# Kernel tuning notes

Measured on AMD Instinct MI355X. Metric: run time of the kernel, lower is better.

The kernel has to match this reference:

```python
import jax, jax.numpy as jnp
import numpy as np

B = 32768
C = 1000


def setup_inputs() -> dict:
    key = jax.random.key(0)
    k1, k2, k3 = jax.random.split(key, 3)
    output = jax.random.normal(k1, (B, C), dtype=jnp.float32)
    target = jax.random.randint(k2, (B,), 0, C, dtype=jnp.int64)
    # loss_lams rows are (approx) probability vectors from the previous epoch
    lams = jax.random.uniform(k3, (C, C), dtype=jnp.float32)
    loss_lams = lams / jnp.sum(lams, axis=1, keepdims=True)
    return {"output": output, "target": target, "loss_lams": loss_lams}


def reference(output, target, loss_lams):
    """OLS loss forward.

    Returns (loss, cur_epoch_lams_update, cur_epoch_cnt_update) where the
    updates are the increments added to the zero-initialized per-epoch state
    (update_loss_lams side effect), and loss = 0.5*CE + 0.5*softCE.
    """
    b, c = output.shape
    target = target.astype(jnp.int32)

    # --- update_loss_lams: softmax, keep samples where argmax == target,
    # scatter-add their prob vectors into the row of their target class ---
    probs = jax.nn.softmax(output, axis=1)                      # [B, C]
    pred = jnp.argmax(probs, axis=1)                            # [B]
    correct = (pred == target).astype(output.dtype)             # [B]
    lams_update = jax.ops.segment_sum(probs * correct[:, None], target,
                                      num_segments=c)           # [C, C]
    cnt_update = jax.ops.segment_sum(correct, target, num_segments=c)  # [C]

    # --- loss: 0.5 * hard CE + 0.5 * soft CE with loss_lams soft labels ---
    log_probs = jax.nn.log_softmax(output, axis=1)              # [B, C]
    ce = -jnp.mean(jnp.take_along_axis(log_probs, target[:, None], axis=1))
    soft_targets = loss_lams[target]                            # [B, C] gather
    soft_ce = -jnp.sum(log_probs * soft_targets) / b
    loss = 0.5 * ce + 0.5 * soft_ce
    return loss, lams_update, cnt_update
```

## Files before the change

kernel.cpp:

```cpp
#include <hip/hip_runtime.h>
#include <math.h>

constexpr int B_ROWS = 32768;
constexpr int C_COLS = 1000;
constexpr int VEC4   = C_COLS / 4;

__global__ __launch_bounds__(256) void ols_loss_kernel(
    const float* __restrict__ output,
    const int*   __restrict__ target,
    const float* __restrict__ lams,
    float*       __restrict__ d_loss,
    float*       __restrict__ lams_upd,
    float*       __restrict__ cnt_upd)
{
    __shared__ float s_loss[4];
    const int lane = threadIdx.x & 63;
    const int wid  = threadIdx.x >> 6;
    const int wavesPerBlock = blockDim.x >> 6;
    const int gwave = blockIdx.x * wavesPerBlock + wid;
    const int nwave = gridDim.x * wavesPerBlock;
    const bool has3 = (lane + 192) < VEC4;

    float lossAcc = 0.0f;

    for (int row = gwave; row < B_ROWS; row += nwave) {
        const float4* xr = reinterpret_cast<const float4*>(output + (size_t)row * C_COLS);
        float4 v0 = xr[lane];
        float4 v1 = xr[lane + 64];
        float4 v2 = xr[lane + 128];
        float4 v3 = has3 ? xr[lane + 192]
                         : make_float4(-INFINITY, -INFINITY, -INFINITY, -INFINITY);

        float m  = v0.x;
        int   am = 4 * lane;
#define OLS_UPD(val, idx) { float _v = (val); if (_v > m) { m = _v; am = (idx); } }
        OLS_UPD(v0.y, 4*lane + 1)  OLS_UPD(v0.z, 4*lane + 2)  OLS_UPD(v0.w, 4*lane + 3)
        OLS_UPD(v1.x, 4*lane + 256) OLS_UPD(v1.y, 4*lane + 257)
        OLS_UPD(v1.z, 4*lane + 258) OLS_UPD(v1.w, 4*lane + 259)
        OLS_UPD(v2.x, 4*lane + 512) OLS_UPD(v2.y, 4*lane + 513)
        OLS_UPD(v2.z, 4*lane + 514) OLS_UPD(v2.w, 4*lane + 515)
        OLS_UPD(v3.x, 4*lane + 768) OLS_UPD(v3.y, 4*lane + 769)
        OLS_UPD(v3.z, 4*lane + 770) OLS_UPD(v3.w, 4*lane + 771)
#undef OLS_UPD

#pragma unroll
        for (int off = 32; off > 0; off >>= 1) {
            float om = __shfl_xor(m, off);
            int   oa = __shfl_xor(am, off);
            if (om > m || (om == m && oa < am)) { m = om; am = oa; }
        }

        float s =
            __expf(v0.x - m) + __expf(v0.y - m) + __expf(v0.z - m) + __expf(v0.w - m) +
            __expf(v1.x - m) + __expf(v1.y - m) + __expf(v1.z - m) + __expf(v1.w - m) +
            __expf(v2.x - m) + __expf(v2.y - m) + __expf(v2.z - m) + __expf(v2.w - m) +
            __expf(v3.x - m) + __expf(v3.y - m) + __expf(v3.z - m) + __expf(v3.w - m);
#pragma unroll
        for (int off = 32; off > 0; off >>= 1) s += __shfl_xor(s, off);

        const float lse = m + __logf(s);

        const int   t   = target[row];
        const float x_t = output[(size_t)row * C_COLS + t];

        const float4* lr = reinterpret_cast<const float4*>(lams + (size_t)t * C_COLS);
        float4 l0 = lr[lane];
        float4 l1 = lr[lane + 64];
        float4 l2 = lr[lane + 128];
        float dot = l0.x*v0.x + l0.y*v0.y + l0.z*v0.z + l0.w*v0.w
                  + l1.x*v1.x + l1.y*v1.y + l1.z*v1.z + l1.w*v1.w
                  + l2.x*v2.x + l2.y*v2.y + l2.z*v2.z + l2.w*v2.w;
        float rs  = l0.x + l0.y + l0.z + l0.w
                  + l1.x + l1.y + l1.z + l1.w
                  + l2.x + l2.y + l2.z + l2.w;
        if (has3) {
            float4 l3 = lr[lane + 192];
            dot += l3.x*v3.x + l3.y*v3.y + l3.z*v3.z + l3.w*v3.w;
            rs  += l3.x + l3.y + l3.z + l3.w;
        }
#pragma unroll
        for (int off = 32; off > 0; off >>= 1) {
            dot += __shfl_xor(dot, off);
            rs  += __shfl_xor(rs,  off);
        }

        if (lane == 0) lossAcc += 0.5f * ((lse - x_t) + (lse * rs - dot));

        if (am == t) {
            const float inv = 1.0f / s;
            float* dst = lams_upd + (size_t)t * C_COLS;
            atomicAdd(&dst[4*lane + 0],   __expf(v0.x - m) * inv);
            atomicAdd(&dst[4*lane + 1],   __expf(v0.y - m) * inv);
            atomicAdd(&dst[4*lane + 2],   __expf(v0.z - m) * inv);
            atomicAdd(&dst[4*lane + 3],   __expf(v0.w - m) * inv);
            atomicAdd(&dst[4*lane + 256], __expf(v1.x - m) * inv);
            atomicAdd(&dst[4*lane + 257], __expf(v1.y - m) * inv);
            atomicAdd(&dst[4*lane + 258], __expf(v1.z - m) * inv);
            atomicAdd(&dst[4*lane + 259], __expf(v1.w - m) * inv);
            atomicAdd(&dst[4*lane + 512], __expf(v2.x - m) * inv);
            atomicAdd(&dst[4*lane + 513], __expf(v2.y - m) * inv);
            atomicAdd(&dst[4*lane + 514], __expf(v2.z - m) * inv);
            atomicAdd(&dst[4*lane + 515], __expf(v2.w - m) * inv);
            if (has3) {
                atomicAdd(&dst[4*lane + 768], __expf(v3.x - m) * inv);
                atomicAdd(&dst[4*lane + 769], __expf(v3.y - m) * inv);
                atomicAdd(&dst[4*lane + 770], __expf(v3.z - m) * inv);
                atomicAdd(&dst[4*lane + 771], __expf(v3.w - m) * inv);
            }
            if (lane == 0) atomicAdd(&cnt_upd[t], 1.0f);
        }
    }

    if (lane == 0) s_loss[wid] = lossAcc;
    __syncthreads();
    if (threadIdx.x == 0) {
        float tot = 0.0f;
        for (int i = 0; i < wavesPerBlock; ++i) tot += s_loss[i];
        atomicAdd(d_loss, tot * (1.0f / (float)B_ROWS));
    }
}

extern "C" void kernel_launch(void* const* d_in, const int* in_sizes, int n_in,
                              void* d_out, int out_size, void* d_ws, size_t ws_size,
                              hipStream_t stream) {
    const float* output = (const float*)d_in[0];
    const int*   target = (const int*)d_in[1];
    const float* lams   = (const float*)d_in[2];

    float* out      = (float*)d_out;
    float* d_loss   = out;
    float* lams_upd = out + 1;
    float* cnt_upd  = out + 1 + C_COLS * C_COLS;

    hipMemsetAsync(d_out, 0, (size_t)out_size * sizeof(float), stream);

    dim3 grid(2048), block(256);
    ols_loss_kernel<<<grid, block, 0, stream>>>(output, target, lams,
                                                d_loss, lams_upd, cnt_upd);
}
```

Measured before the change: 211.6 us.

## Map one row per wave, issue all loads upfront, fetch target logit via shuffle

Replaces the grid-stride loop with one row per wave and a grid of B/4 blocks. The target and lams-row loads are issued before the max reduction so they overlap with the logits loads. Logits use nontemporal loads. The three reductions (sum, dot, rowsum) share one fused shuffle loop, and x_t comes from a register shuffle instead of a dependent global load. This removes serialized load latency per row, at the cost of launching 8192 blocks and one atomic on the loss per block.

New measurement: 275.8 us. 30.3% more time.

```diff
diff --git a/kernel.cpp b/kernel.cpp
--- a/kernel.cpp
+++ b/kernel.cpp
@@ -4,6 +4,8 @@
 constexpr int B_ROWS = 32768;
 constexpr int C_COLS = 1000;
 constexpr int VEC4   = C_COLS / 4;
+
+using f4 = __attribute__((ext_vector_type(4))) float;
 
 __global__ __launch_bounds__(256) void ols_loss_kernel(
     const float* __restrict__ output,
@@ -16,106 +18,106 @@
     __shared__ float s_loss[4];
     const int lane = threadIdx.x & 63;
     const int wid  = threadIdx.x >> 6;
-    const int wavesPerBlock = blockDim.x >> 6;
-    const int gwave = blockIdx.x * wavesPerBlock + wid;
-    const int nwave = gridDim.x * wavesPerBlock;
-    const bool has3 = (lane + 192) < VEC4;
+    const int row  = blockIdx.x * 4 + wid;
+    const bool has3 = lane < (VEC4 - 192);
 
-    float lossAcc = 0.0f;
+    const int t = __builtin_nontemporal_load(target + row);
 
-    for (int row = gwave; row < B_ROWS; row += nwave) {
-        const float4* xr = reinterpret_cast<const float4*>(output + (size_t)row * C_COLS);
-        float4 v0 = xr[lane];
-        float4 v1 = xr[lane + 64];
-        float4 v2 = xr[lane + 128];
-        float4 v3 = has3 ? xr[lane + 192]
-                         : make_float4(-INFINITY, -INFINITY, -INFINITY, -INFINITY);
+    const f4* xr = reinterpret_cast<const f4*>(output + (size_t)row * C_COLS);
+    f4 v0 = __builtin_nontemporal_load(xr + lane);
+    f4 v1 = __builtin_nontemporal_load(xr + lane + 64);
+    f4 v2 = __builtin_nontemporal_load(xr + lane + 128);
+    f4 v3;
+    if (has3) v3 = __builtin_nontemporal_load(xr + lane + 192);
+    else      v3 = (f4){-INFINITY, -INFINITY, -INFINITY, -INFINITY};
 
-        float m  = v0.x;
-        int   am = 4 * lane;
+    const f4* lr = reinterpret_cast<const f4*>(lams + (size_t)t * C_COLS);
+    f4 l0 = lr[lane];
+    f4 l1 = lr[lane + 64];
+    f4 l2 = lr[lane + 128];
+    f4 l3;
+    if (has3) l3 = lr[lane + 192];
+    else      l3 = (f4){0.0f, 0.0f, 0.0f, 0.0f};
+
+    float m  = v0[0];
+    int   am = 4 * lane;
 #define OLS_UPD(val, idx) { float _v = (val); if (_v > m) { m = _v; am = (idx); } }
-        OLS_UPD(v0.y, 4*lane + 1)  OLS_UPD(v0.z, 4*lane + 2)  OLS_UPD(v0.w, 4*lane + 3)
-        OLS_UPD(v1.x, 4*lane + 256) OLS_UPD(v1.y, 4*lane + 257)
-        OLS_UPD(v1.z, 4*lane + 258) OLS_UPD(v1.w, 4*lane + 259)
-        OLS_UPD(v2.x, 4*lane + 512) OLS_UPD(v2.y, 4*lane + 513)
-        OLS_UPD(v2.z, 4*lane + 514) OLS_UPD(v2.w, 4*lane + 515)
-        OLS_UPD(v3.x, 4*lane + 768) OLS_UPD(v3.y, 4*lane + 769)
-        OLS_UPD(v3.z, 4*lane + 770) OLS_UPD(v3.w, 4*lane + 771)
+    OLS_UPD(v0[1], 4*lane + 1)   OLS_UPD(v0[2], 4*lane + 2)   OLS_UPD(v0[3], 4*lane + 3)
+    OLS_UPD(v1[0], 4*lane + 256) OLS_UPD(v1[1], 4*lane + 257)
+    OLS_UPD(v1[2], 4*lane + 258) OLS_UPD(v1[3], 4*lane + 259)
+    OLS_UPD(v2[0], 4*lane + 512) OLS_UPD(v2[1], 4*lane + 513)
+    OLS_UPD(v2[2], 4*lane + 514) OLS_UPD(v2[3], 4*lane + 515)
+    OLS_UPD(v3[0], 4*lane + 768) OLS_UPD(v3[1], 4*lane + 769)
+    OLS_UPD(v3[2], 4*lane + 770) OLS_UPD(v3[3], 4*lane + 771)
 #undef OLS_UPD
 
 #pragma unroll
-        for (int off = 32; off > 0; off >>= 1) {
-            float om = __shfl_xor(m, off);
-            int   oa = __shfl_xor(am, off);
-            if (om > m || (om == m && oa < am)) { m = om; am = oa; }
-        }
-
-        float s =
-            __expf(v0.x - m) + __expf(v0.y - m) + __expf(v0.z - m) + __expf(v0.w - m) +
-            __expf(v1.x - m) + __expf(v1.y - m) + __expf(v1.z - m) + __expf(v1.w - m) +
-            __expf(v2.x - m) + __expf(v2.y - m) + __expf(v2.z - m) + __expf(v2.w - m) +
-            __expf(v3.x - m) + __expf(v3.y - m) + __expf(v3.z - m) + __expf(v3.w - m);
-#pragma unroll
-        for (int off = 32; off > 0; off >>= 1) s += __shfl_xor(s, off);
-
-        const float lse = m + __logf(s);
-
-        const int   t   = target[row];
-        const float x_t = output[(size_t)row * C_COLS + t];
-
-        const float4* lr = reinterpret_cast<const float4*>(lams + (size_t)t * C_COLS);
-        float4 l0 = lr[lane];
-        float4 l1 = lr[lane + 64];
-        float4 l2 = lr[lane + 128];
-        float dot = l0.x*v0.x + l0.y*v0.y + l0.z*v0.z + l0.w*v0.w
-                  + l1.x*v1.x + l1.y*v1.y + l1.z*v1.z + l1.w*v1.w
-                  + l2.x*v2.x + l2.y*v2.y + l2.z*v2.z + l2.w*v2.w;
-        float rs  = l0.x + l0.y + l0.z + l0.w
-                  + l1.x + l1.y + l1.z + l1.w
-                  + l2.x + l2.y + l2.z + l2.w;
-        if (has3) {
-            float4 l3 = lr[lane + 192];
-            dot += l3.x*v3.x + l3.y*v3.y + l3.z*v3.z + l3.w*v3.w;
-            rs  += l3.x + l3.y + l3.z + l3.w;
-        }
-#pragma unroll
-        for (int off = 32; off > 0; off >>= 1) {
-            dot += __shfl_xor(dot, off);
-            rs  += __shfl_xor(rs,  off);
-        }
-
-        if (lane == 0) lossAcc += 0.5f * ((lse - x_t) + (lse * rs - dot));
-
-        if (am == t) {
-            const float inv = 1.0f / s;
-            float* dst = lams_upd + (size_t)t * C_COLS;
-            atomicAdd(&dst[4*lane + 0],   __expf(v0.x - m) * inv);
-            atomicAdd(&dst[4*lane + 1],   __expf(v0.y - m) * inv);
-            atomicAdd(&dst[4*lane + 2],   __expf(v0.z - m) * inv);
-            atomicAdd(&dst[4*lane + 3],   __expf(v0.w - m) * inv);
-            atomicAdd(&dst[4*lane + 256], __expf(v1.x - m) * inv);
-            atomicAdd(&dst[4*lane + 257], __expf(v1.y - m) * inv);
-            atomicAdd(&dst[4*lane + 258], __expf(v1.z - m) * inv);
-            atomicAdd(&dst[4*lane + 259], __expf(v1.w - m) * inv);
-            atomicAdd(&dst[4*lane + 512], __expf(v2.x - m) * inv);
-            atomicAdd(&dst[4*lane + 513], __expf(v2.y - m) * inv);
-            atomicAdd(&dst[4*lane + 514], __expf(v2.z - m) * inv);
-            atomicAdd(&dst[4*lane + 515], __expf(v2.w - m) * inv);
-            if (has3) {
-                atomicAdd(&dst[4*lane + 768], __expf(v3.x - m) * inv);
-                atomicAdd(&dst[4*lane + 769], __expf(v3.y - m) * inv);
-                atomicAdd(&dst[4*lane + 770], __expf(v3.z - m) * inv);
-                atomicAdd(&dst[4*lane + 771], __expf(v3.w - m) * inv);
-            }
-            if (lane == 0) atomicAdd(&cnt_upd[t], 1.0f);
-        }
+    for (int off = 32; off > 0; off >>= 1) {
+        float om = __shfl_xor(m, off);
+        int   oa = __shfl_xor(am, off);
+        if (om > m || (om == m && oa < am)) { m = om; am = oa; }
     }
 
-    if (lane == 0) s_loss[wid] = lossAcc;
+    float dot = l0[0]*v0[0] + l0[1]*v0[1] + l0[2]*v0[2] + l0[3]*v0[3]
+              + l1[0]*v1[0] + l1[1]*v1[1] + l1[2]*v1[2] + l1[3]*v1[3]
+              + l2[0]*v2[0] + l2[1]*v2[1] + l2[2]*v2[2] + l2[3]*v2[3];
+    float rs  = l0[0] + l0[1] + l0[2] + l0[3]
+              + l1[0] + l1[1] + l1[2] + l1[3]
+              + l2[0] + l2[1] + l2[2] + l2[3];
+    if (has3) {
+        dot += l3[0]*v3[0] + l3[1]*v3[1] + l3[2]*v3[2] + l3[3]*v3[3];
+        rs  += l3[0] + l3[1] + l3[2] + l3[3];
+    }
+
+    float s =
+        __expf(v0[0] - m) + __expf(v0[1] - m) + __expf(v0[2] - m) + __expf(v0[3] - m) +
+        __expf(v1[0] - m) + __expf(v1[1] - m) + __expf(v1[2] - m) + __expf(v1[3] - m) +
+        __expf(v2[0] - m) + __expf(v2[1] - m) + __expf(v2[2] - m) + __expf(v2[3] - m) +
+        __expf(v3[0] - m) + __expf(v3[1] - m) + __expf(v3[2] - m) + __expf(v3[3] - m);
+
+#pragma unroll
+    for (int off = 32; off > 0; off >>= 1) {
+        s   += __shfl_xor(s,   off);
+        dot += __shfl_xor(dot, off);
+        rs  += __shfl_xor(rs,  off);
+    }
+
+    const float lse = m + __logf(s);
+
+    const int g = t >> 8, e = t & 3, src_lane = (t >> 2) & 63;
+    f4 vg = (g == 0) ? v0 : (g == 1) ? v1 : (g == 2) ? v2 : v3;
+    float ce = (e == 0) ? vg[0] : (e == 1) ? vg[1] : (e == 2) ? vg[2] : vg[3];
+    const float x_t = __shfl(ce, src_lane, 64);
+
+    if (lane == 0) s_loss[wid] = 0.5f * ((lse - x_t) + (lse * rs - dot));
+
+    if (am == t) {
+        const float inv = 1.0f / s;
+        float* dst = lams_upd + (size_t)t * C_COLS;
+        atomicAdd(&dst[4*lane + 0],   __expf(v0[0] - m) * inv);
+        atomicAdd(&dst[4*lane + 1],   __expf(v0[1] - m) * inv);
+        atomicAdd(&dst[4*lane + 2],   __expf(v0[2] - m) * inv);
+        atomicAdd(&dst[4*lane + 3],   __expf(v0[3] - m) * inv);
+        atomicAdd(&dst[4*lane + 256], __expf(v1[0] - m) * inv);
+        atomicAdd(&dst[4*lane + 257], __expf(v1[1] - m) * inv);
+        atomicAdd(&dst[4*lane + 258], __expf(v1[2] - m) * inv);
+        atomicAdd(&dst[4*lane + 259], __expf(v1[3] - m) * inv);
+        atomicAdd(&dst[4*lane + 512], __expf(v2[0] - m) * inv);
+        atomicAdd(&dst[4*lane + 513], __expf(v2[1] - m) * inv);
+        atomicAdd(&dst[4*lane + 514], __expf(v2[2] - m) * inv);
+        atomicAdd(&dst[4*lane + 515], __expf(v2[3] - m) * inv);
+        if (has3) {
+            atomicAdd(&dst[4*lane + 768], __expf(v3[0] - m) * inv);
+            atomicAdd(&dst[4*lane + 769], __expf(v3[1] - m) * inv);
+            atomicAdd(&dst[4*lane + 770], __expf(v3[2] - m) * inv);
+            atomicAdd(&dst[4*lane + 771], __expf(v3[3] - m) * inv);
+        }
+        if (lane == 0) atomicAdd(&cnt_upd[t], 1.0f);
+    }
+
     __syncthreads();
     if (threadIdx.x == 0) {
-        float tot = 0.0f;
-        for (int i = 0; i < wavesPerBlock; ++i) tot += s_loss[i];
+        float tot = (s_loss[0] + s_loss[1]) + (s_loss[2] + s_loss[3]);
         atomicAdd(d_loss, tot * (1.0f / (float)B_ROWS));
     }
 }
@@ -134,7 +136,7 @@
 
     hipMemsetAsync(d_out, 0, (size_t)out_size * sizeof(float), stream);
 
-    dim3 grid(2048), block(256);
+    dim3 grid(B_ROWS / 4), block(256);
     ols_loss_kernel<<<grid, block, 0, stream>>>(output, target, lams,
                                                 d_loss, lams_upd, cnt_upd);
 }
```
